# Optimization experiments

Measured on AMD Instinct MI355X. Metric: run time of the kernel, lower is better.

Reference implementation:

```python
import jax, jax.numpy as jnp
import numpy as np

LN_EPS = 1e-5

def _layernorm(x, g, b):
    mu = jnp.mean(x, axis=-1, keepdims=True)
    var = jnp.mean(jnp.square(x - mu), axis=-1, keepdims=True)
    return (x - mu) * jax.lax.rsqrt(var + LN_EPS) * g + b

def setup_inputs() -> dict:
    key = jax.random.key(0)
    B, IN_DIM, S, D = 16384, 512, 32, 128
    ks = jax.random.split(key, 6)
    return {
        "x": jax.random.normal(ks[0], (B, IN_DIM), dtype=jnp.float32),
        "memory": jax.random.normal(ks[1], (1, S, D), dtype=jnp.float32),
        "ln_g": jnp.ones((IN_DIM,), dtype=jnp.float32),
        "ln_b": jnp.zeros((IN_DIM,), dtype=jnp.float32),
        "w_in": jax.random.normal(ks[2], (IN_DIM, D), dtype=jnp.float32) * 0.02,
        "b_in": jnp.zeros((D,), dtype=jnp.float32),
        "w_gate": jax.random.normal(ks[3], (2 * D, D), dtype=jnp.float32) * 0.02,
        "b_gate": jnp.zeros((D,), dtype=jnp.float32),
    }

def reference(x, memory, ln_g, ln_b, w_in, b_in, w_gate, b_gate):
    B = x.shape[0]
    mem = memory[0]                                   # [S, D]
    S, D = mem.shape
    x_proj = _layernorm(x, ln_g, ln_b) @ w_in + b_in  # [B, D]
    scores = x_proj @ mem.T                           # [B, S]
    probs = jax.nn.softmax(scores, axis=-1)           # [B, S]
    # read path
    read_content = probs @ mem                        # [B, D]
    # write path
    mem_b = jnp.broadcast_to(mem, (B, S, D))
    xp_b = jnp.broadcast_to(x_proj[:, None, :], (B, S, D))
    gate_in = jnp.concatenate([mem_b, xp_b], axis=-1)              # [B, S, 2D]
    update_gate = jax.nn.sigmoid(gate_in @ w_gate + b_gate)        # [B, S, D]
    write_info = probs[:, :, None] * x_proj[:, None, :]            # [B, S, D]
    avg_gate = jnp.mean(update_gate, axis=0, keepdims=True)        # [1, S, D]
    avg_write = jnp.mean(write_info, axis=0, keepdims=True)        # [1, S, D]
    new_memory = memory * (1.0 - avg_gate) + avg_write * avg_gate  # [1, S, D]
    return read_content, jax.lax.stop_gradient(new_memory)
```

## Files before the change

kernel.cpp:

```cpp
#include <hip/hip_runtime.h>
#include <stdint.h>

typedef __attribute__((ext_vector_type(8))) short bfrag_t;
typedef __attribute__((ext_vector_type(4))) float floatx4;

#define WFRAG_OFF   0
#define GB_OFF      294912
#define BU_OFF      311296
#define BS_OFF      311808
#define MEMFRAG_OFF 311936
#define ACC_OFF     327680

#define M_XPF   0
#define M_U     8192
#define M_SC    24576
#define M_PR    28672
#define M_PRT   30720
#define M_RC    32768
#define M_LDS   49152

__device__ __forceinline__ unsigned short f2bf(float f) {
    unsigned u = __float_as_uint(f);
    u += 0x7fffu + ((u >> 16) & 1u);
    return (unsigned short)(u >> 16);
}
__device__ __forceinline__ float sigm(float v) {
    return __builtin_amdgcn_rcpf(1.0f + __expf(-v));
}
__device__ __forceinline__ void writefrag(unsigned short* wf, int k, int n, float v) {
    int kt = k >> 5, kk = k & 31;
    int lane = (n & 15) | ((kk >> 3) << 4);
    wf[(((kt * 18) + (n >> 4)) * 64 + lane) * 8 + (kk & 7)] = f2bf(v);
}

__global__ __launch_bounds__(256) void prep_kernel(
    const float* __restrict__ memv, const float* __restrict__ w_in,
    const float* __restrict__ b_in, const float* __restrict__ w_gate,
    const float* __restrict__ b_gate, unsigned char* __restrict__ ws, int ncopy)
{
    int bid = blockIdx.x, t = threadIdx.x;
    unsigned short* wfrag = (unsigned short*)(ws + WFRAG_OFF);
    const float* wg2 = w_gate + 128 * 128;

    if (bid < 256) {
        __shared__ float wrow[2][128];
        int k0 = bid * 2;
        wrow[t >> 7][t & 127] = w_in[(size_t)(k0 + (t >> 7)) * 128 + (t & 127)];
        __syncthreads();
        for (int kl = 0; kl < 2; ++kl) {
            int k = k0 + kl;
            float v;
            if (t < 128) {
                v = wrow[kl][t];
            } else {
                int d = t - 128;
                float acc = 0.f;
                #pragma unroll 16
                for (int j = 0; j < 128; ++j) acc += wrow[kl][j] * wg2[j * 128 + d];
                v = acc;
            }
            writefrag(wfrag, k, t, v);
            if (t < 32) {
                float acc = 0.f;
                #pragma unroll 16
                for (int d = 0; d < 128; ++d) acc += wrow[kl][d] * memv[t * 128 + d];
                writefrag(wfrag, k, 256 + t, acc);
            }
        }
    } else if (bid < 272) {
        int idx = (bid - 256) * 256 + t;
        int s = idx >> 7, d = idx & 127;
        float acc = b_gate[d];
        #pragma unroll 16
        for (int k = 0; k < 128; ++k) acc += memv[s * 128 + k] * w_gate[k * 128 + d];
        ((float*)(ws + GB_OFF))[idx] = acc;
    } else if (bid == 272) {
        if (t < 128) {
            float acc = 0.f;
            #pragma unroll 16
            for (int j = 0; j < 128; ++j) acc += b_in[j] * wg2[j * 128 + t];
            ((float*)(ws + BU_OFF))[t] = acc;
        }
        if (t < 32) {
            float acc = 0.f;
            #pragma unroll 16
            for (int d = 0; d < 128; ++d) acc += b_in[d] * memv[t * 128 + d];
            ((float*)(ws + BS_OFF))[t] = acc;
        }
        unsigned short* mfr = (unsigned short*)(ws + MEMFRAG_OFF);
        for (int idx = t; idx < 4096; idx += 256) {
            int s = idx >> 7, d = idx & 127;
            mfr[((d >> 4) * 64 + ((d & 15) | (((s >> 3) & 3) << 4))) * 8 + (s & 7)]
                = f2bf(memv[idx]);
        }
    } else {
        int zb = bid - 273;
        float4* dst = (float4*)(ws + ACC_OFF + (size_t)zb * ncopy * 2048);
        int n4 = ncopy * 128;
        for (int i = t; i < n4; i += 256) dst[i] = (float4){0.f, 0.f, 0.f, 0.f};
    }
}

__global__ __launch_bounds__(512, 4) void main_kernel(
    const float* __restrict__ x,
    const float* __restrict__ ln_g, const float* __restrict__ ln_b,
    const float* __restrict__ b_in, unsigned char* __restrict__ ws,
    float* __restrict__ out, int copy_mask)
{
    __shared__ char smem[M_LDS] __attribute__((aligned(16)));

    int tid = threadIdx.x;
    int w = tid >> 6, l = tid & 63;
    int lane_lo = l & 15, lane_hi = l >> 4;
    int row_base = blockIdx.x * 32;

    const float4* x4 = (const float4*)x;
    float4 g0 = ((const float4*)ln_g)[l];
    float4 g1 = ((const float4*)ln_g)[l + 64];
    float4 q0 = ((const float4*)ln_b)[l];
    float4 q1 = ((const float4*)ln_b)[l + 64];
    #pragma unroll
    for (int i = 0; i < 4; ++i) {
        int r = w * 4 + i;
        float4 xa = x4[(size_t)(row_base + r) * 128 + l];
        float4 xb = x4[(size_t)(row_base + r) * 128 + 64 + l];
        float s1 = xa.x + xa.y + xa.z + xa.w + xb.x + xb.y + xb.z + xb.w;
        float s2 = xa.x*xa.x + xa.y*xa.y + xa.z*xa.z + xa.w*xa.w
                 + xb.x*xb.x + xb.y*xb.y + xb.z*xb.z + xb.w*xb.w;
        #pragma unroll
        for (int m = 1; m < 64; m <<= 1) {
            s1 += __shfl_xor(s1, m);
            s2 += __shfl_xor(s2, m);
        }
        float mu = s1 * (1.f / 512.f);
        float var = s2 * (1.f / 512.f) - mu * mu;
        float rs = rsqrtf(var + 1e-5f);
        float ya0 = (xa.x - mu) * rs * g0.x + q0.x;
        float ya1 = (xa.y - mu) * rs * g0.y + q0.y;
        float ya2 = (xa.z - mu) * rs * g0.z + q0.z;
        float ya3 = (xa.w - mu) * rs * g0.w + q0.w;
        float yb0 = (xb.x - mu) * rs * g1.x + q1.x;
        float yb1 = (xb.y - mu) * rs * g1.y + q1.y;
        float yb2 = (xb.z - mu) * rs * g1.z + q1.z;
        float yb3 = (xb.w - mu) * rs * g1.w + q1.w;
        unsigned long long pa =
            (unsigned long long)f2bf(ya0) | ((unsigned long long)f2bf(ya1) << 16) |
            ((unsigned long long)f2bf(ya2) << 32) | ((unsigned long long)f2bf(ya3) << 48);
        unsigned long long pb =
            (unsigned long long)f2bf(yb0) | ((unsigned long long)f2bf(yb1) << 16) |
            ((unsigned long long)f2bf(yb2) << 32) | ((unsigned long long)f2bf(yb3) << 48);
        int sw = (r & 7) << 4;
        *(unsigned long long*)(smem + ((r * 1024 + l * 8) ^ sw)) = pa;
        *(unsigned long long*)(smem + ((r * 1024 + 512 + l * 8) ^ sw)) = pb;
    }
    __syncthreads();

    int nf = (w < 2) ? 3 : 2;
    int nts[3] = {w, w + 8, 16 + w};

    const bfrag_t* wf = (const bfrag_t*)(ws + WFRAG_OFF);
    int swa = (l & 7) << 4;
    int ab0 = lane_lo * 1024 + (lane_hi << 4);
    int ab1 = (16 + lane_lo) * 1024 + (lane_hi << 4);

    floatx4 acc[3][2];
    #pragma unroll
    for (int i = 0; i < 3; ++i)
        #pragma unroll
        for (int mt = 0; mt < 2; ++mt)
            acc[i][mt] = (floatx4){0.f, 0.f, 0.f, 0.f};

    bfrag_t acur0, acur1, anxt0, anxt1, bcur[3], bnxt[3];
    acur0 = *(const bfrag_t*)(smem + (ab0 ^ swa));
    acur1 = *(const bfrag_t*)(smem + (ab1 ^ swa));
    #pragma unroll
    for (int i = 0; i < 3; ++i)
        if (i < nf) bcur[i] = wf[(0 * 18 + nts[i]) * 64 + l];

    for (int kt = 0; kt < 16; ++kt) {
        if (kt < 15) {
            int ko = (kt + 1) * 64;
            anxt0 = *(const bfrag_t*)(smem + ((ab0 + ko) ^ swa));
            anxt1 = *(const bfrag_t*)(smem + ((ab1 + ko) ^ swa));
            #pragma unroll
            for (int i = 0; i < 3; ++i)
                if (i < nf) bnxt[i] = wf[((kt + 1) * 18 + nts[i]) * 64 + l];
        }
        #pragma unroll
        for (int i = 0; i < 3; ++i) {
            if (i < nf) {
                acc[i][0] = __builtin_amdgcn_mfma_f32_16x16x32_bf16(acur0, bcur[i], acc[i][0], 0, 0, 0);
                acc[i][1] = __builtin_amdgcn_mfma_f32_16x16x32_bf16(acur1, bcur[i], acc[i][1], 0, 0, 0);
            }
        }
        acur0 = anxt0; acur1 = anxt1;
        #pragma unroll
        for (int i = 0; i < 3; ++i)
            if (i < nf) bcur[i] = bnxt[i];
    }
    __syncthreads();

    {
        const float* bu = (const float*)(ws + BU_OFF);
        const float* bs = (const float*)(ws + BS_OFF);
        #pragma unroll
        for (int i = 0; i < 3; ++i) {
            if (i < nf) {
                int n = nts[i] * 16 + lane_lo;
                #pragma unroll
                for (int mt = 0; mt < 2; ++mt) {
                    #pragma unroll
                    for (int r4 = 0; r4 < 4; ++r4) {
                        int row = mt * 16 + lane_hi * 4 + r4;
                        float v = acc[i][mt][r4];
                        if (i == 0) {
                            float val = v + b_in[n];
                            int addr = M_XPF +
                                (((n >> 4) * 64 + ((n & 15) | ((row >> 3) << 4))) * 8
                                 + (row & 7)) * 2;
                            *(unsigned short*)(smem + addr) = f2bf(val);
                        } else if (i == 1) {
                            int d = n - 128;
                            *(float*)(smem + M_U + (row * 128 + d) * 4) = v + bu[d];
                        } else {
                            int s = n - 256;
                            *(float*)(smem + M_SC + (row * 32 + s) * 4) = v + bs[s];
                        }
                    }
                }
            }
        }
    }
    __syncthreads();

    #pragma unroll
    for (int i = 0; i < 4; ++i) {
        int r = w * 4 + i;
        int s = l & 31;
        float sc = *(const float*)(smem + M_SC + (r * 32 + s) * 4);
        float mx = sc;
        #pragma unroll
        for (int m = 1; m < 32; m <<= 1) mx = fmaxf(mx, __shfl_xor(mx, m));
        float e = __expf(sc - mx);
        float sum = e;
        #pragma unroll
        for (int m = 1; m < 32; m <<= 1) sum += __shfl_xor(sum, m);
        float p = e * __builtin_amdgcn_rcpf(sum);
        if (l < 32) {
            unsigned short pb = f2bf(p);
            *(unsigned short*)(smem + M_PR +
                (((r >> 4) * 64 + ((r & 15) + 16 * (s >> 3))) * 8 + (s & 7)) * 2) = pb;
            *(unsigned short*)(smem + M_PRT +
                (((s >> 4) * 64 + ((s & 15) + 16 * (r >> 3))) * 8 + (r & 7)) * 2) = pb;
        }
    }
    __syncthreads();

    float* accw = (float*)(ws + ACC_OFF + (size_t)(blockIdx.x & copy_mask) * 32768);
    float* accg = accw + 4096;

    {
        bfrag_t pa0 = *(const bfrag_t*)(smem + M_PR + l * 16);
        bfrag_t pa1 = *(const bfrag_t*)(smem + M_PR + 1024 + l * 16);
        bfrag_t pat0 = *(const bfrag_t*)(smem + M_PRT + l * 16);
        bfrag_t pat1 = *(const bfrag_t*)(smem + M_PRT + 1024 + l * 16);
        bfrag_t bm = ((const bfrag_t*)(ws + MEMFRAG_OFF))[w * 64 + l];
        bfrag_t bx = *(const bfrag_t*)(smem + M_XPF + (w * 64 + l) * 16);

        floatx4 r0 = (floatx4){0.f, 0.f, 0.f, 0.f};
        floatx4 r1 = (floatx4){0.f, 0.f, 0.f, 0.f};
        r0 = __builtin_amdgcn_mfma_f32_16x16x32_bf16(pa0, bm, r0, 0, 0, 0);
        r1 = __builtin_amdgcn_mfma_f32_16x16x32_bf16(pa1, bm, r1, 0, 0, 0);
        floatx4 w0 = (floatx4){0.f, 0.f, 0.f, 0.f};
        floatx4 w1 = (floatx4){0.f, 0.f, 0.f, 0.f};
        w0 = __builtin_amdgcn_mfma_f32_16x16x32_bf16(pat0, bx, w0, 0, 0, 0);
        w1 = __builtin_amdgcn_mfma_f32_16x16x32_bf16(pat1, bx, w1, 0, 0, 0);

        int nc = w * 16 + lane_lo;
        #pragma unroll
        for (int r4 = 0; r4 < 4; ++r4) {
            int row = lane_hi * 4 + r4;
            *(float*)(smem + M_RC + (row * 128 + nc) * 4) = r0[r4];
            *(float*)(smem + M_RC + ((row + 16) * 128 + nc) * 4) = r1[r4];
            __hip_atomic_fetch_add(&accw[row * 128 + nc], w0[r4],
                                   __ATOMIC_RELAXED, __HIP_MEMORY_SCOPE_AGENT);
            __hip_atomic_fetch_add(&accw[(row + 16) * 128 + nc], w1[r4],
                                   __ATOMIC_RELAXED, __HIP_MEMORY_SCOPE_AGENT);
        }
    }
    __syncthreads();

    {
        const float4* rc4 = (const float4*)(smem + M_RC);
        float4* out4 = (float4*)out;
        #pragma unroll
        for (int q = 0; q < 2; ++q) {
            int idx = q * 512 + tid;
            int row = idx >> 5, c4 = idx & 31;
            out4[(size_t)(row_base + row) * 32 + c4] = rc4[idx];
        }
    }
    {
        int sbase = w * 4;
        const float* gb = (const float*)(ws + GB_OFF);
        float gbr0[4], gbr1[4], ag0[4], ag1[4];
        #pragma unroll
        for (int si = 0; si < 4; ++si) {
            gbr0[si] = gb[(sbase + si) * 128 + l];
            gbr1[si] = gb[(sbase + si) * 128 + l + 64];
            ag0[si] = 0.f; ag1[si] = 0.f;
        }
        for (int r = 0; r < 32; ++r) {
            float uv0 = *(const float*)(smem + M_U + (r * 128 + l) * 4);
            float uv1 = *(const float*)(smem + M_U + (r * 128 + l + 64) * 4);
            #pragma unroll
            for (int si = 0; si < 4; ++si) {
                ag0[si] += sigm(gbr0[si] + uv0);
                ag1[si] += sigm(gbr1[si] + uv1);
            }
        }
        #pragma unroll
        for (int si = 0; si < 4; ++si) {
            __hip_atomic_fetch_add(&accg[(sbase + si) * 128 + l],      ag0[si],
                                   __ATOMIC_RELAXED, __HIP_MEMORY_SCOPE_AGENT);
            __hip_atomic_fetch_add(&accg[(sbase + si) * 128 + l + 64], ag1[si],
                                   __ATOMIC_RELAXED, __HIP_MEMORY_SCOPE_AGENT);
        }
    }
}

__global__ __launch_bounds__(512) void fin_kernel(
    const float* __restrict__ memv, const unsigned char* __restrict__ ws,
    float* __restrict__ out2, int ncopy)
{
    int i = blockIdx.x * 512 + threadIdx.x;
    const float* base = (const float*)(ws + ACC_OFF);
    float aw = 0.f, ag = 0.f;
    #pragma unroll 8
    for (int c = 0; c < ncopy; ++c) {
        aw += base[c * 8192 + i];
        ag += base[c * 8192 + 4096 + i];
    }
    ag *= (1.f / 16384.f);
    aw *= (1.f / 16384.f);
    out2[i] = memv[i] * (1.f - ag) + aw * ag;
}

extern "C" void kernel_launch(void* const* d_in, const int* in_sizes, int n_in,
                              void* d_out, int out_size, void* d_ws, size_t ws_size,
                              hipStream_t stream)
{
    (void)in_sizes; (void)n_in; (void)out_size;
    const float* x      = (const float*)d_in[0];
    const float* memv   = (const float*)d_in[1];
    const float* ln_g   = (const float*)d_in[2];
    const float* ln_b   = (const float*)d_in[3];
    const float* w_in   = (const float*)d_in[4];
    const float* b_in   = (const float*)d_in[5];
    const float* w_gate = (const float*)d_in[6];
    const float* b_gate = (const float*)d_in[7];
    float* out = (float*)d_out;
    unsigned char* ws = (unsigned char*)d_ws;

    int ncopy = (ws_size >= (size_t)ACC_OFF + 64 * 32768) ? 64 : 32;

    hipLaunchKernelGGL(prep_kernel, dim3(289), dim3(256), 0, stream,
                       memv, w_in, b_in, w_gate, b_gate, ws, ncopy);
    hipLaunchKernelGGL(main_kernel, dim3(512), dim3(512), 0, stream,
                       x, ln_g, ln_b, b_in, ws, out, ncopy - 1);
    hipLaunchKernelGGL(fin_kernel, dim3(8), dim3(512), 0, stream,
                       memv, ws, out + 2097152, ncopy);
}
```

Before: 49.30 us.

## Replace atomic accumulation with per-block partial sums and parallel final reduction

Each main_kernel block now writes its write-info and gate partial sums to its own slot in workspace, replacing the relaxed atomic adds into shared copies. That removes the zeroing blocks from the prep kernel. fin_kernel now reduces 512 partials per element across 64 blocks through a shared-memory tree. Read-content is stored directly to global from the MFMA fragments instead of being staged through LDS. The A tile gets its own LDS region so a barrier can be dropped, which grows LDS to 64KB and lowers occupancy to 2 blocks per CU. It also assumes the workspace holds 512 partial slots of 32KB each, about 16MB, and no longer checks ws_size.

```diff
diff --git a/kernel.cpp b/kernel.cpp
--- a/kernel.cpp
+++ b/kernel.cpp
@@ -10,14 +10,15 @@
 #define BS_OFF      311808
 #define MEMFRAG_OFF 311936
 #define ACC_OFF     327680
-
-#define M_XPF   0
-#define M_U     8192
-#define M_SC    24576
-#define M_PR    28672
-#define M_PRT   30720
-#define M_RC    32768
-#define M_LDS   49152
+#define NBLK        512
+
+#define M_A     0
+#define M_XPF   32768
+#define M_U     40960
+#define M_SC    57344
+#define M_PR    61440
+#define M_PRT   63488
+#define M_LDS   65536
 
 __device__ __forceinline__ unsigned short f2bf(float f) {
     unsigned u = __float_as_uint(f);
@@ -36,7 +37,7 @@
 __global__ __launch_bounds__(256) void prep_kernel(
     const float* __restrict__ memv, const float* __restrict__ w_in,
     const float* __restrict__ b_in, const float* __restrict__ w_gate,
-    const float* __restrict__ b_gate, unsigned char* __restrict__ ws, int ncopy)
+    const float* __restrict__ b_gate, unsigned char* __restrict__ ws)
 {
     int bid = blockIdx.x, t = threadIdx.x;
     unsigned short* wfrag = (unsigned short*)(ws + WFRAG_OFF);
@@ -74,7 +75,7 @@
         #pragma unroll 16
         for (int k = 0; k < 128; ++k) acc += memv[s * 128 + k] * w_gate[k * 128 + d];
         ((float*)(ws + GB_OFF))[idx] = acc;
-    } else if (bid == 272) {
+    } else {
         if (t < 128) {
             float acc = 0.f;
             #pragma unroll 16
@@ -93,19 +94,14 @@
             mfr[((d >> 4) * 64 + ((d & 15) | (((s >> 3) & 3) << 4))) * 8 + (s & 7)]
                 = f2bf(memv[idx]);
         }
-    } else {
-        int zb = bid - 273;
-        float4* dst = (float4*)(ws + ACC_OFF + (size_t)zb * ncopy * 2048);
-        int n4 = ncopy * 128;
-        for (int i = t; i < n4; i += 256) dst[i] = (float4){0.f, 0.f, 0.f, 0.f};
-    }
-}
-
-__global__ __launch_bounds__(512, 4) void main_kernel(
+    }
+}
+
+__global__ __launch_bounds__(512, 2) void main_kernel(
     const float* __restrict__ x,
     const float* __restrict__ ln_g, const float* __restrict__ ln_b,
     const float* __restrict__ b_in, unsigned char* __restrict__ ws,
-    float* __restrict__ out, int copy_mask)
+    float* __restrict__ out)
 {
     __shared__ char smem[M_LDS] __attribute__((aligned(16)));
 
@@ -150,8 +146,8 @@
             (unsigned long long)f2bf(yb0) | ((unsigned long long)f2bf(yb1) << 16) |
             ((unsigned long long)f2bf(yb2) << 32) | ((unsigned long long)f2bf(yb3) << 48);
         int sw = (r & 7) << 4;
-        *(unsigned long long*)(smem + ((r * 1024 + l * 8) ^ sw)) = pa;
-        *(unsigned long long*)(smem + ((r * 1024 + 512 + l * 8) ^ sw)) = pb;
+        *(unsigned long long*)(smem + M_A + ((r * 1024 + l * 8) ^ sw)) = pa;
+        *(unsigned long long*)(smem + M_A + ((r * 1024 + 512 + l * 8) ^ sw)) = pb;
     }
     __syncthreads();
 
@@ -171,8 +167,8 @@
             acc[i][mt] = (floatx4){0.f, 0.f, 0.f, 0.f};
 
     bfrag_t acur0, acur1, anxt0, anxt1, bcur[3], bnxt[3];
-    acur0 = *(const bfrag_t*)(smem + (ab0 ^ swa));
-    acur1 = *(const bfrag_t*)(smem + (ab1 ^ swa));
+    acur0 = *(const bfrag_t*)(smem + M_A + (ab0 ^ swa));
+    acur1 = *(const bfrag_t*)(smem + M_A + (ab1 ^ swa));
     #pragma unroll
     for (int i = 0; i < 3; ++i)
         if (i < nf) bcur[i] = wf[(0 * 18 + nts[i]) * 64 + l];
@@ -180,8 +176,8 @@
     for (int kt = 0; kt < 16; ++kt) {
         if (kt < 15) {
             int ko = (kt + 1) * 64;
-            anxt0 = *(const bfrag_t*)(smem + ((ab0 + ko) ^ swa));
-            anxt1 = *(const bfrag_t*)(smem + ((ab1 + ko) ^ swa));
+            anxt0 = *(const bfrag_t*)(smem + M_A + ((ab0 + ko) ^ swa));
+            anxt1 = *(const bfrag_t*)(smem + M_A + ((ab1 + ko) ^ swa));
             #pragma unroll
             for (int i = 0; i < 3; ++i)
                 if (i < nf) bnxt[i] = wf[((kt + 1) * 18 + nts[i]) * 64 + l];
@@ -198,7 +194,6 @@
         for (int i = 0; i < 3; ++i)
             if (i < nf) bcur[i] = bnxt[i];
     }
-    __syncthreads();
 
     {
         const float* bu = (const float*)(ws + BU_OFF);
@@ -256,9 +251,7 @@
     }
     __syncthreads();
 
-    float* accw = (float*)(ws + ACC_OFF + (size_t)(blockIdx.x & copy_mask) * 32768);
-    float* accg = accw + 4096;
-
+    float* pw = (float*)(ws + ACC_OFF + (size_t)blockIdx.x * 32768);
     {
         bfrag_t pa0 = *(const bfrag_t*)(smem + M_PR + l * 16);
         bfrag_t pa1 = *(const bfrag_t*)(smem + M_PR + 1024 + l * 16);
@@ -280,29 +273,17 @@
         #pragma unroll
         for (int r4 = 0; r4 < 4; ++r4) {
             int row = lane_hi * 4 + r4;
-            *(float*)(smem + M_RC + (row * 128 + nc) * 4) = r0[r4];
-            *(float*)(smem + M_RC + ((row + 16) * 128 + nc) * 4) = r1[r4];
-            __hip_atomic_fetch_add(&accw[row * 128 + nc], w0[r4],
-                                   __ATOMIC_RELAXED, __HIP_MEMORY_SCOPE_AGENT);
-            __hip_atomic_fetch_add(&accw[(row + 16) * 128 + nc], w1[r4],
-                                   __ATOMIC_RELAXED, __HIP_MEMORY_SCOPE_AGENT);
-        }
-    }
-    __syncthreads();
-
-    {
-        const float4* rc4 = (const float4*)(smem + M_RC);
-        float4* out4 = (float4*)out;
-        #pragma unroll
-        for (int q = 0; q < 2; ++q) {
-            int idx = q * 512 + tid;
-            int row = idx >> 5, c4 = idx & 31;
-            out4[(size_t)(row_base + row) * 32 + c4] = rc4[idx];
-        }
-    }
+            out[(size_t)(row_base + row) * 128 + nc] = r0[r4];
+            out[(size_t)(row_base + row + 16) * 128 + nc] = r1[r4];
+            pw[row * 128 + nc] = w0[r4];
+            pw[(row + 16) * 128 + nc] = w1[r4];
+        }
+    }
+
     {
         int sbase = w * 4;
         const float* gb = (const float*)(ws + GB_OFF);
+        float* pg = pw + 4096;
         float gbr0[4], gbr1[4], ag0[4], ag1[4];
         #pragma unroll
         for (int si = 0; si < 4; ++si) {
@@ -321,36 +302,47 @@
         }
         #pragma unroll
         for (int si = 0; si < 4; ++si) {
-            __hip_atomic_fetch_add(&accg[(sbase + si) * 128 + l],      ag0[si],
-                                   __ATOMIC_RELAXED, __HIP_MEMORY_SCOPE_AGENT);
-            __hip_atomic_fetch_add(&accg[(sbase + si) * 128 + l + 64], ag1[si],
-                                   __ATOMIC_RELAXED, __HIP_MEMORY_SCOPE_AGENT);
+            pg[(sbase + si) * 128 + l]      = ag0[si];
+            pg[(sbase + si) * 128 + l + 64] = ag1[si];
         }
     }
 }
 
 __global__ __launch_bounds__(512) void fin_kernel(
     const float* __restrict__ memv, const unsigned char* __restrict__ ws,
-    float* __restrict__ out2, int ncopy)
+    float* __restrict__ out2)
 {
-    int i = blockIdx.x * 512 + threadIdx.x;
+    __shared__ float red[2][8][64];
+    int b = blockIdx.x, t = threadIdx.x;
+    int el = t & 63, ch = t >> 6;
     const float* base = (const float*)(ws + ACC_OFF);
+    int e = b * 64 + el;
+
     float aw = 0.f, ag = 0.f;
     #pragma unroll 8
-    for (int c = 0; c < ncopy; ++c) {
-        aw += base[c * 8192 + i];
-        ag += base[c * 8192 + 4096 + i];
-    }
-    ag *= (1.f / 16384.f);
-    aw *= (1.f / 16384.f);
-    out2[i] = memv[i] * (1.f - ag) + aw * ag;
+    for (int c = ch * 64; c < ch * 64 + 64; ++c) {
+        aw += base[(size_t)c * 8192 + e];
+        ag += base[(size_t)c * 8192 + 4096 + e];
+    }
+    red[0][ch][el] = aw;
+    red[1][ch][el] = ag;
+    __syncthreads();
+    if (t < 64) {
+        float a = 0.f, g = 0.f;
+        #pragma unroll
+        for (int c = 0; c < 8; ++c) { a += red[0][c][t]; g += red[1][c][t]; }
+        a *= (1.f / 16384.f);
+        g *= (1.f / 16384.f);
+        int i = b * 64 + t;
+        out2[i] = memv[i] * (1.f - g) + a * g;
+    }
 }
 
 extern "C" void kernel_launch(void* const* d_in, const int* in_sizes, int n_in,
                               void* d_out, int out_size, void* d_ws, size_t ws_size,
                               hipStream_t stream)
 {
-    (void)in_sizes; (void)n_in; (void)out_size;
+    (void)in_sizes; (void)n_in; (void)out_size; (void)ws_size;
     const float* x      = (const float*)d_in[0];
     const float* memv   = (const float*)d_in[1];
     const float* ln_g   = (const float*)d_in[2];
@@ -362,12 +354,10 @@
     float* out = (float*)d_out;
     unsigned char* ws = (unsigned char*)d_ws;
 
-    int ncopy = (ws_size >= (size_t)ACC_OFF + 64 * 32768) ? 64 : 32;
-
-    hipLaunchKernelGGL(prep_kernel, dim3(289), dim3(256), 0, stream,
-                       memv, w_in, b_in, w_gate, b_gate, ws, ncopy);
-    hipLaunchKernelGGL(main_kernel, dim3(512), dim3(512), 0, stream,
-                       x, ln_g, ln_b, b_in, ws, out, ncopy - 1);
-    hipLaunchKernelGGL(fin_kernel, dim3(8), dim3(512), 0, stream,
-                       memv, ws, out + 2097152, ncopy);
-}
+    hipLaunchKernelGGL(prep_kernel, dim3(273), dim3(256), 0, stream,
+                       memv, w_in, b_in, w_gate, b_gate, ws);
+    hipLaunchKernelGGL(main_kernel, dim3(NBLK), dim3(512), 0, stream,
+                       x, ln_g, ln_b, b_in, ws, out);
+    hipLaunchKernelGGL(fin_kernel, dim3(64), dim3(512), 0, stream,
+                       memv, ws, out + 2097152);
+}
```

Measured after the change: 62.02 us. +25.8%, slower.
